# Kernel tuning notes

Hardware: AMD Instinct MI355X
Metric: run time of the kernel (lower is better)

The kernel has to match this reference:

```python
import jax, jax.numpy as jnp
import numpy as np

SIGMA = 0.1  # kernel-point influence radius (KPConv linear correlation)


def setup_inputs() -> dict:
    key = jax.random.key(0)
    k1, k2, k3, k4, k5 = jax.random.split(key, 5)
    N, K, KP, CIN, COUT = 65536, 32, 15, 64, 128
    pos = jax.random.uniform(k1, (N, 3), dtype=jnp.float32)
    feats = jax.random.normal(k2, (N, CIN), dtype=jnp.float32)
    kernel_points = jax.random.normal(k3, (KP, 3), dtype=jnp.float32) * 0.05
    weights = jax.random.normal(k4, (KP, CIN, COUT), dtype=jnp.float32) / np.sqrt(KP * CIN)
    neighbors = jax.random.randint(k5, (N, K), 0, N, dtype=jnp.int64)
    return {"pos": pos, "feats": feats, "kernel_points": kernel_points,
            "weights": weights, "neighbors": neighbors}


def reference(pos, feats, kernel_points, weights, neighbors):
    # pos: [N,3], feats: [N,Cin], kernel_points: [Kp,3],
    # weights: [Kp,Cin,Cout], neighbors: [N,K] int
    neigh_pos = pos[neighbors]                      # [N,K,3] irregular gather
    rel = neigh_pos - pos[:, None, :]               # [N,K,3]
    # distance from each relative neighbor offset to each kernel point
    d = rel[:, :, None, :] - kernel_points[None, None, :, :]   # [N,K,Kp,3]
    dist = jnp.sqrt(jnp.sum(d * d, axis=-1))        # [N,K,Kp]
    infl = jnp.maximum(0.0, 1.0 - dist / SIGMA)     # linear correlation
    neigh_feat = feats[neighbors]                   # [N,K,Cin] irregular gather
    # per-kernel-point weighted neighbor aggregation, then projection
    weighted = jnp.einsum('njk,njc->nkc', infl, neigh_feat)    # [N,Kp,Cin]
    out = jnp.einsum('nkc,kcd->nd', weighted, weights)         # [N,Cout]
    return out
```

## Files before the change

### kernel.cpp

```cpp
#include <hip/hip_runtime.h>

#define NPTS  65536
#define KNB   32
#define KPn   15
#define CIN   64
#define COUT  128
#define MPTS  16
#define THREADS 256
#define TPB   4
#define WSTRIDE 968
#define BCAP  48
#define RCAP  96
#define NTILE 8
#define KSTEPS 30
#define WELEMS (NTILE * KSTEPS * 64 * 8)

typedef __attribute__((ext_vector_type(8))) short short8;
typedef __attribute__((ext_vector_type(4))) float f32x4;

__device__ __forceinline__ unsigned int f2bf(float f) {
    union { float f; unsigned int i; } v; v.f = f;
    return (v.i + 0x7fffu + ((v.i >> 16) & 1u)) >> 16;
}

__global__ void wtrans_kernel(const float* __restrict__ w,
                              const float* __restrict__ kpts,
                              unsigned short* __restrict__ wTf,
                              float4* __restrict__ kpq_out) {
    const int d = blockIdx.x * 256 + threadIdx.x;
    if (d < WELEMS) {
        const int j    = d & 7;
        const int lane = (d >> 3) & 63;
        const int ks   = (d >> 9) % KSTEPS;
        const int t    = d / (KSTEPS * 512);
        const int f    = ks * 32 + (lane >> 4) * 8 + j;
        const int cg   = f / 120;
        const int rem  = f - cg * 120;
        const int orig = (rem >> 3) * 64 + cg * 8 + (rem & 7);
        const int n    = t * 16 + (lane & 15);
        wTf[d] = (unsigned short)f2bf(w[(size_t)orig * COUT + n]);
    }
    if (blockIdx.x == 0 && threadIdx.x < 16) {
        const int k = threadIdx.x;
        if (k < KPn) {
            const float x = kpts[k * 3 + 0];
            const float y = kpts[k * 3 + 1];
            const float z = kpts[k * 3 + 2];
            kpq_out[k] = make_float4(x, y, z, x * x + y * y + z * z);
        } else {
            float mx = 0.f;
            for (int i = 0; i < KPn; ++i) {
                const float x = kpts[i * 3 + 0];
                const float y = kpts[i * 3 + 1];
                const float z = kpts[i * 3 + 2];
                mx = fmaxf(mx, x * x + y * y + z * z);
            }
            const float R = 0.1f + sqrtf(mx);
            kpq_out[15] = make_float4(R * R, 0.f, 0.f, 0.f);
        }
    }
}

__global__ __launch_bounds__(THREADS, 4) void kpconv_kernel(
    const float* __restrict__ pos,
    const float* __restrict__ feats,
    const unsigned short* __restrict__ wTf,
    const float4* __restrict__ kpq_in,
    const int*   __restrict__ neighbors,
    float*       __restrict__ out)
{
    __shared__ unsigned short wl[MPTS * WSTRIDE];
    __shared__ unsigned int  bpk[MPTS][BCAP];
    __shared__ int    bcnt[MPTS];
    __shared__ float  cposf[MPTS * 3];
    __shared__ float4 kpq[KPn];
    __shared__ float  rlx[RCAP], rly[RCAP], rlz[RCAP], rld[RCAP];
    __shared__ unsigned int rsl[RCAP];
    __shared__ int    nact;
    __shared__ float  R2s;

    const int tid = threadIdx.x;

    if (tid < KPn) kpq[tid] = kpq_in[tid];
    if (tid == KPn) R2s = kpq_in[15].x;

    for (int t8 = 0; t8 < TPB; ++t8) {
        const int n0 = (blockIdx.x * TPB + t8) * MPTS;

        if (tid < MPTS) bcnt[tid] = 0;
        if (tid == THREADS - 1) nact = 0;
        if (tid < MPTS * 3) cposf[tid] = pos[(size_t)n0 * 3 + tid];
        __syncthreads();

        {
            const float R2 = R2s;
            #pragma unroll
            for (int it = 0; it < 2; ++it) {
                const int s  = tid + it * THREADS;
                const int p  = s >> 5;
                const int nb = neighbors[(size_t)n0 * KNB + s];
                const float rx = pos[(size_t)nb * 3 + 0] - cposf[p * 3 + 0];
                const float ry = pos[(size_t)nb * 3 + 1] - cposf[p * 3 + 1];
                const float rz = pos[(size_t)nb * 3 + 2] - cposf[p * 3 + 2];
                const float d2r = rx * rx + ry * ry + rz * rz;
                if (d2r < R2) {
                    const int idx = atomicAdd(&nact, 1);
                    if (idx < RCAP) {
                        rlx[idx] = rx; rly[idx] = ry; rlz[idx] = rz; rld[idx] = d2r;
                        rsl[idx] = ((unsigned int)p << 16) | (unsigned int)nb;
                    }
                }
            }
        }
        __syncthreads();

        {
            const int E = min(nact, RCAP);
            for (int u = tid; u < E * 16; u += THREADS) {
                const int e = u >> 4;
                const int k = u & 15;
                if (k < KPn) {
                    const float4 kp  = kpq[k];
                    const float  d2r = rld[e];
                    const float dot = rlx[e] * kp.x + rly[e] * kp.y + rlz[e] * kp.z;
                    if (dot > 0.5f * (d2r - 0.01f + kp.w)) {
                        const float d2 = fmaxf(d2r - 2.f * dot + kp.w, 0.f);
                        const float w  = 1.0f - 10.0f * sqrtf(d2);
                        const unsigned int wq = (unsigned int)(w * 4095.0f + 0.5f);
                        const unsigned int sl = rsl[e];
                        const int p = (int)(sl >> 16);
                        const int idx = atomicAdd(&bcnt[p], 1);
                        if (idx < BCAP)
                            bpk[p][idx] = ((sl & 0xFFFFu) << 16) |
                                          ((unsigned int)k << 12) | wq;
                    }
                }
            }
        }
        __syncthreads();

        #pragma unroll
        for (int it = 0; it < 8; ++it) {
            const int wi = tid + it * THREADS;
            const int cg = wi & 7;
            const int k  = (wi >> 3) & 15;
            const int p  = wi >> 7;
            if (k < KPn) {
                float a0=0.f,a1=0.f,a2=0.f,a3=0.f,a4=0.f,a5=0.f,a6=0.f,a7=0.f;
                const int cnt = min(bcnt[p], BCAP);
                for (int e = 0; e < cnt; ++e) {
                    const unsigned int id = bpk[p][e];
                    if (((id >> 12) & 15u) == (unsigned int)k) {
                        const float wv = (float)(id & 4095u) * (1.0f / 4095.0f);
                        const float* fr = feats + (size_t)(id >> 16) * CIN + cg * 8;
                        const float4 f0 = *(const float4*)fr;
                        const float4 f1 = *(const float4*)(fr + 4);
                        a0 += wv * f0.x; a1 += wv * f0.y; a2 += wv * f0.z; a3 += wv * f0.w;
                        a4 += wv * f1.x; a5 += wv * f1.y; a6 += wv * f1.z; a7 += wv * f1.w;
                    }
                }
                uint4 u;
                u.x = f2bf(a0) | (f2bf(a1) << 16);
                u.y = f2bf(a2) | (f2bf(a3) << 16);
                u.z = f2bf(a4) | (f2bf(a5) << 16);
                u.w = f2bf(a6) | (f2bf(a7) << 16);
                *(uint4*)(wl + p * WSTRIDE + cg * 120 + k * 8) = u;
            }
        }
        __syncthreads();

        {
            const int wave = tid >> 6;
            const int lane = tid & 63;
            const int m    = lane & 15;
            const int q    = lane >> 4;

            f32x4 acc0 = {0.f, 0.f, 0.f, 0.f};
            f32x4 acc1 = {0.f, 0.f, 0.f, 0.f};

            const unsigned short* ap = wl + m * WSTRIDE + q * 8;
            const short8* bp0 = (const short8*)wTf + (size_t)(2 * wave) * KSTEPS * 64 + lane;
            const short8* bp1 = bp0 + (size_t)KSTEPS * 64;

            #pragma unroll 5
            for (int ks = 0; ks < KSTEPS; ++ks, ap += 32) {
                const short8 a  = *(const short8*)ap;
                const short8 b0 = bp0[ks * 64];
                const short8 b1 = bp1[ks * 64];
                acc0 = __builtin_amdgcn_mfma_f32_16x16x32_bf16(a, b0, acc0, 0, 0, 0);
                acc1 = __builtin_amdgcn_mfma_f32_16x16x32_bf16(a, b1, acc1, 0, 0, 0);
            }

            const int nb0 = wave * 32;
            #pragma unroll
            for (int r = 0; r < 4; ++r) {
                const size_t row = (size_t)(n0 + q * 4 + r) * COUT;
                out[row + nb0 + m]      = acc0[r];
                out[row + nb0 + 16 + m] = acc1[r];
            }
        }
    }
}

extern "C" void kernel_launch(void* const* d_in, const int* in_sizes, int n_in,
                              void* d_out, int out_size, void* d_ws, size_t ws_size,
                              hipStream_t stream) {
    const float* pos       = (const float*)d_in[0];
    const float* feats     = (const float*)d_in[1];
    const float* kpts      = (const float*)d_in[2];
    const float* weights   = (const float*)d_in[3];
    const int*   neighbors = (const int*)d_in[4];
    float*       out       = (float*)d_out;
    unsigned short* wTf    = (unsigned short*)d_ws;
    float4* kpq            = (float4*)((char*)d_ws + WELEMS * 2);

    wtrans_kernel<<<(WELEMS + 255) / 256, 256, 0, stream>>>(weights, kpts, wTf, kpq);
    kpconv_kernel<<<NPTS / (MPTS * TPB), THREADS, 0, stream>>>(
        pos, feats, wTf, kpq, neighbors, out);
}
```

Before: 145.3 us.

## Process 32 points per block in one pass instead of looping over 16-point tiles

Removes the per-block loop over four 16-point tiles. Each block now handles 32 points once, with 2048 blocks instead of 1024, and the candidate buffer capacity is raised to match. In the MFMA stage each wave computes two M-tiles, so every B fragment loaded from global weights is reused across 32 rows instead of 16. This halves weight traffic per point, but LDS use per block roughly doubles and the launch-bounds occupancy hint drops from 4 to 2.

Measured after the change: 160.1 us. 10.2% more time.

```diff
diff --git a/kernel.cpp b/kernel.cpp
--- a/kernel.cpp
+++ b/kernel.cpp
@@ -5,12 +5,11 @@
 #define KPn   15
 #define CIN   64
 #define COUT  128
-#define MPTS  16
+#define MPTS  32
 #define THREADS 256
-#define TPB   4
 #define WSTRIDE 968
 #define BCAP  48
-#define RCAP  96
+#define RCAP  160
 #define NTILE 8
 #define KSTEPS 30
 #define WELEMS (NTILE * KSTEPS * 64 * 8)
@@ -61,7 +60,7 @@
     }
 }
 
-__global__ __launch_bounds__(THREADS, 4) void kpconv_kernel(
+__global__ __launch_bounds__(THREADS, 2) void kpconv_kernel(
     const float* __restrict__ pos,
     const float* __restrict__ feats,
     const unsigned short* __restrict__ wTf,
@@ -80,124 +79,129 @@
     __shared__ float  R2s;
 
     const int tid = threadIdx.x;
+    const int n0  = blockIdx.x * MPTS;
 
     if (tid < KPn) kpq[tid] = kpq_in[tid];
     if (tid == KPn) R2s = kpq_in[15].x;
-
-    for (int t8 = 0; t8 < TPB; ++t8) {
-        const int n0 = (blockIdx.x * TPB + t8) * MPTS;
-
-        if (tid < MPTS) bcnt[tid] = 0;
-        if (tid == THREADS - 1) nact = 0;
-        if (tid < MPTS * 3) cposf[tid] = pos[(size_t)n0 * 3 + tid];
-        __syncthreads();
-
-        {
-            const float R2 = R2s;
-            #pragma unroll
-            for (int it = 0; it < 2; ++it) {
-                const int s  = tid + it * THREADS;
-                const int p  = s >> 5;
-                const int nb = neighbors[(size_t)n0 * KNB + s];
-                const float rx = pos[(size_t)nb * 3 + 0] - cposf[p * 3 + 0];
-                const float ry = pos[(size_t)nb * 3 + 1] - cposf[p * 3 + 1];
-                const float rz = pos[(size_t)nb * 3 + 2] - cposf[p * 3 + 2];
-                const float d2r = rx * rx + ry * ry + rz * rz;
-                if (d2r < R2) {
-                    const int idx = atomicAdd(&nact, 1);
-                    if (idx < RCAP) {
-                        rlx[idx] = rx; rly[idx] = ry; rlz[idx] = rz; rld[idx] = d2r;
-                        rsl[idx] = ((unsigned int)p << 16) | (unsigned int)nb;
-                    }
+    if (tid < MPTS) bcnt[tid] = 0;
+    if (tid == THREADS - 1) nact = 0;
+    if (tid < MPTS * 3) cposf[tid] = pos[(size_t)n0 * 3 + tid];
+    __syncthreads();
+
+    {
+        const float R2 = R2s;
+        #pragma unroll
+        for (int it = 0; it < MPTS * KNB / THREADS; ++it) {
+            const int s  = tid + it * THREADS;
+            const int p  = s >> 5;
+            const int nb = neighbors[(size_t)n0 * KNB + s];
+            const float rx = pos[(size_t)nb * 3 + 0] - cposf[p * 3 + 0];
+            const float ry = pos[(size_t)nb * 3 + 1] - cposf[p * 3 + 1];
+            const float rz = pos[(size_t)nb * 3 + 2] - cposf[p * 3 + 2];
+            const float d2r = rx * rx + ry * ry + rz * rz;
+            if (d2r < R2) {
+                const int idx = atomicAdd(&nact, 1);
+                if (idx < RCAP) {
+                    rlx[idx] = rx; rly[idx] = ry; rlz[idx] = rz; rld[idx] = d2r;
+                    rsl[idx] = ((unsigned int)p << 16) | (unsigned int)nb;
                 }
             }
         }
-        __syncthreads();
-
-        {
-            const int E = min(nact, RCAP);
-            for (int u = tid; u < E * 16; u += THREADS) {
-                const int e = u >> 4;
-                const int k = u & 15;
-                if (k < KPn) {
-                    const float4 kp  = kpq[k];
-                    const float  d2r = rld[e];
-                    const float dot = rlx[e] * kp.x + rly[e] * kp.y + rlz[e] * kp.z;
-                    if (dot > 0.5f * (d2r - 0.01f + kp.w)) {
-                        const float d2 = fmaxf(d2r - 2.f * dot + kp.w, 0.f);
-                        const float w  = 1.0f - 10.0f * sqrtf(d2);
-                        const unsigned int wq = (unsigned int)(w * 4095.0f + 0.5f);
-                        const unsigned int sl = rsl[e];
-                        const int p = (int)(sl >> 16);
-                        const int idx = atomicAdd(&bcnt[p], 1);
-                        if (idx < BCAP)
-                            bpk[p][idx] = ((sl & 0xFFFFu) << 16) |
-                                          ((unsigned int)k << 12) | wq;
-                    }
+    }
+    __syncthreads();
+
+    {
+        const int E = min(nact, RCAP);
+        for (int u = tid; u < E * 16; u += THREADS) {
+            const int e = u >> 4;
+            const int k = u & 15;
+            if (k < KPn) {
+                const float4 kp  = kpq[k];
+                const float  d2r = rld[e];
+                const float dot = rlx[e] * kp.x + rly[e] * kp.y + rlz[e] * kp.z;
+                if (dot > 0.5f * (d2r - 0.01f + kp.w)) {
+                    const float d2 = fmaxf(d2r - 2.f * dot + kp.w, 0.f);
+                    const float w  = 1.0f - 10.0f * sqrtf(d2);
+                    const unsigned int wq = (unsigned int)(w * 4095.0f + 0.5f);
+                    const unsigned int sl = rsl[e];
+                    const int p = (int)(sl >> 16);
+                    const int idx = atomicAdd(&bcnt[p], 1);
+                    if (idx < BCAP)
+                        bpk[p][idx] = ((sl & 0xFFFFu) << 16) |
+                                      ((unsigned int)k << 12) | wq;
                 }
             }
         }
-        __syncthreads();
-
+    }
+    __syncthreads();
+
+    #pragma unroll
+    for (int it = 0; it < 16; ++it) {
+        const int wi = tid + it * THREADS;
+        const int cg = wi & 7;
+        const int k  = (wi >> 3) & 15;
+        const int p  = wi >> 7;
+        if (k < KPn) {
+            float a0=0.f,a1=0.f,a2=0.f,a3=0.f,a4=0.f,a5=0.f,a6=0.f,a7=0.f;
+            const int cnt = min(bcnt[p], BCAP);
+            for (int e = 0; e < cnt; ++e) {
+                const unsigned int id = bpk[p][e];
+                if (((id >> 12) & 15u) == (unsigned int)k) {
+                    const float wv = (float)(id & 4095u) * (1.0f / 4095.0f);
+                    const float* fr = feats + (size_t)(id >> 16) * CIN + cg * 8;
+                    const float4 f0 = *(const float4*)fr;
+                    const float4 f1 = *(const float4*)(fr + 4);
+                    a0 += wv * f0.x; a1 += wv * f0.y; a2 += wv * f0.z; a3 += wv * f0.w;
+                    a4 += wv * f1.x; a5 += wv * f1.y; a6 += wv * f1.z; a7 += wv * f1.w;
+                }
+            }
+            uint4 u;
+            u.x = f2bf(a0) | (f2bf(a1) << 16);
+            u.y = f2bf(a2) | (f2bf(a3) << 16);
+            u.z = f2bf(a4) | (f2bf(a5) << 16);
+            u.w = f2bf(a6) | (f2bf(a7) << 16);
+            *(uint4*)(wl + p * WSTRIDE + cg * 120 + k * 8) = u;
+        }
+    }
+    __syncthreads();
+
+    {
+        const int wave = tid >> 6;
+        const int lane = tid & 63;
+        const int m    = lane & 15;
+        const int q    = lane >> 4;
+
+        f32x4 acc00 = {0.f,0.f,0.f,0.f};
+        f32x4 acc01 = {0.f,0.f,0.f,0.f};
+        f32x4 acc10 = {0.f,0.f,0.f,0.f};
+        f32x4 acc11 = {0.f,0.f,0.f,0.f};
+
+        const unsigned short* a0p = wl + m * WSTRIDE + q * 8;
+        const unsigned short* a1p = a0p + 16 * WSTRIDE;
+        const short8* bp0 = (const short8*)wTf + (size_t)(2 * wave) * KSTEPS * 64 + lane;
+        const short8* bp1 = bp0 + (size_t)KSTEPS * 64;
+
+        #pragma unroll 5
+        for (int ks = 0; ks < KSTEPS; ++ks, a0p += 32, a1p += 32) {
+            const short8 a0 = *(const short8*)a0p;
+            const short8 a1 = *(const short8*)a1p;
+            const short8 b0 = bp0[ks * 64];
+            const short8 b1 = bp1[ks * 64];
+            acc00 = __builtin_amdgcn_mfma_f32_16x16x32_bf16(a0, b0, acc00, 0, 0, 0);
+            acc01 = __builtin_amdgcn_mfma_f32_16x16x32_bf16(a0, b1, acc01, 0, 0, 0);
+            acc10 = __builtin_amdgcn_mfma_f32_16x16x32_bf16(a1, b0, acc10, 0, 0, 0);
+            acc11 = __builtin_amdgcn_mfma_f32_16x16x32_bf16(a1, b1, acc11, 0, 0, 0);
+        }
+
+        const int c0 = 2 * wave * 16 + m;
         #pragma unroll
-        for (int it = 0; it < 8; ++it) {
-            const int wi = tid + it * THREADS;
-            const int cg = wi & 7;
-            const int k  = (wi >> 3) & 15;
-            const int p  = wi >> 7;
-            if (k < KPn) {
-                float a0=0.f,a1=0.f,a2=0.f,a3=0.f,a4=0.f,a5=0.f,a6=0.f,a7=0.f;
-                const int cnt = min(bcnt[p], BCAP);
-                for (int e = 0; e < cnt; ++e) {
-                    const unsigned int id = bpk[p][e];
-                    if (((id >> 12) & 15u) == (unsigned int)k) {
-                        const float wv = (float)(id & 4095u) * (1.0f / 4095.0f);
-                        const float* fr = feats + (size_t)(id >> 16) * CIN + cg * 8;
-                        const float4 f0 = *(const float4*)fr;
-                        const float4 f1 = *(const float4*)(fr + 4);
-                        a0 += wv * f0.x; a1 += wv * f0.y; a2 += wv * f0.z; a3 += wv * f0.w;
-                        a4 += wv * f1.x; a5 += wv * f1.y; a6 += wv * f1.z; a7 += wv * f1.w;
-                    }
-                }
-                uint4 u;
-                u.x = f2bf(a0) | (f2bf(a1) << 16);
-                u.y = f2bf(a2) | (f2bf(a3) << 16);
-                u.z = f2bf(a4) | (f2bf(a5) << 16);
-                u.w = f2bf(a6) | (f2bf(a7) << 16);
-                *(uint4*)(wl + p * WSTRIDE + cg * 120 + k * 8) = u;
-            }
-        }
-        __syncthreads();
-
-        {
-            const int wave = tid >> 6;
-            const int lane = tid & 63;
-            const int m    = lane & 15;
-            const int q    = lane >> 4;
-
-            f32x4 acc0 = {0.f, 0.f, 0.f, 0.f};
-            f32x4 acc1 = {0.f, 0.f, 0.f, 0.f};
-
-            const unsigned short* ap = wl + m * WSTRIDE + q * 8;
-            const short8* bp0 = (const short8*)wTf + (size_t)(2 * wave) * KSTEPS * 64 + lane;
-            const short8* bp1 = bp0 + (size_t)KSTEPS * 64;
-
-            #pragma unroll 5
-            for (int ks = 0; ks < KSTEPS; ++ks, ap += 32) {
-                const short8 a  = *(const short8*)ap;
-                const short8 b0 = bp0[ks * 64];
-                const short8 b1 = bp1[ks * 64];
-                acc0 = __builtin_amdgcn_mfma_f32_16x16x32_bf16(a, b0, acc0, 0, 0, 0);
-                acc1 = __builtin_amdgcn_mfma_f32_16x16x32_bf16(a, b1, acc1, 0, 0, 0);
-            }
-
-            const int nb0 = wave * 32;
-            #pragma unroll
-            for (int r = 0; r < 4; ++r) {
-                const size_t row = (size_t)(n0 + q * 4 + r) * COUT;
-                out[row + nb0 + m]      = acc0[r];
-                out[row + nb0 + 16 + m] = acc1[r];
-            }
+        for (int r = 0; r < 4; ++r) {
+            const size_t row0 = (size_t)(n0 + q * 4 + r) * COUT;
+            const size_t row1 = (size_t)(n0 + 16 + q * 4 + r) * COUT;
+            out[row0 + c0]      = acc00[r];
+            out[row0 + c0 + 16] = acc01[r];
+            out[row1 + c0]      = acc10[r];
+            out[row1 + c0 + 16] = acc11[r];
         }
     }
 }
@@ -215,6 +219,6 @@
     float4* kpq            = (float4*)((char*)d_ws + WELEMS * 2);
 
     wtrans_kernel<<<(WELEMS + 255) / 256, 256, 0, stream>>>(weights, kpts, wTf, kpq);
-    kpconv_kernel<<<NPTS / (MPTS * TPB), THREADS, 0, stream>>>(
+    kpconv_kernel<<<NPTS / MPTS, THREADS, 0, stream>>>(
         pos, feats, wTf, kpq, neighbors, out);
 }
```

## Use 512-thread blocks, one 16-point tile per block, one MFMA tile per wave

Applied to the files above, without the earlier changes.

The kernel stops looping over 4 point tiles per block. Each block now handles a single 16-point tile with 512 threads, launching 4x more blocks, and each of the 8 waves computes one 16-column output tile instead of two. The aim is more parallelism and latency hiding across the gather and MFMA phases, and removing the serial per-tile loop. In exchange the kpq setup is repeated per block, there is more block launch overhead, and each wave has less MFMA work to amortize its A-fragment LDS loads.

Result: faster. 138.2 us (-4.9%).

```diff
diff --git a/kernel.cpp b/kernel.cpp
--- a/kernel.cpp
+++ b/kernel.cpp
@@ -6,8 +6,7 @@
 #define CIN   64
 #define COUT  128
 #define MPTS  16
-#define THREADS 256
-#define TPB   4
+#define THREADS 512
 #define WSTRIDE 968
 #define BCAP  48
 #define RCAP  96
@@ -61,7 +60,7 @@
     }
 }
 
-__global__ __launch_bounds__(THREADS, 4) void kpconv_kernel(
+__global__ __launch_bounds__(THREADS, 8) void kpconv_kernel(
     const float* __restrict__ pos,
     const float* __restrict__ feats,
     const unsigned short* __restrict__ wTf,
@@ -80,125 +79,110 @@
     __shared__ float  R2s;
 
     const int tid = threadIdx.x;
+    const int n0  = blockIdx.x * MPTS;
 
     if (tid < KPn) kpq[tid] = kpq_in[tid];
     if (tid == KPn) R2s = kpq_in[15].x;
-
-    for (int t8 = 0; t8 < TPB; ++t8) {
-        const int n0 = (blockIdx.x * TPB + t8) * MPTS;
-
-        if (tid < MPTS) bcnt[tid] = 0;
-        if (tid == THREADS - 1) nact = 0;
-        if (tid < MPTS * 3) cposf[tid] = pos[(size_t)n0 * 3 + tid];
-        __syncthreads();
-
-        {
-            const float R2 = R2s;
-            #pragma unroll
-            for (int it = 0; it < 2; ++it) {
-                const int s  = tid + it * THREADS;
-                const int p  = s >> 5;
-                const int nb = neighbors[(size_t)n0 * KNB + s];
-                const float rx = pos[(size_t)nb * 3 + 0] - cposf[p * 3 + 0];
-                const float ry = pos[(size_t)nb * 3 + 1] - cposf[p * 3 + 1];
-                const float rz = pos[(size_t)nb * 3 + 2] - cposf[p * 3 + 2];
-                const float d2r = rx * rx + ry * ry + rz * rz;
-                if (d2r < R2) {
-                    const int idx = atomicAdd(&nact, 1);
-                    if (idx < RCAP) {
-                        rlx[idx] = rx; rly[idx] = ry; rlz[idx] = rz; rld[idx] = d2r;
-                        rsl[idx] = ((unsigned int)p << 16) | (unsigned int)nb;
-                    }
+    if (tid < MPTS) bcnt[tid] = 0;
+    if (tid == THREADS - 1) nact = 0;
+    if (tid < MPTS * 3) cposf[tid] = pos[(size_t)n0 * 3 + tid];
+    __syncthreads();
+
+    {
+        const float R2 = R2s;
+        const int s  = tid;
+        const int p  = s >> 5;
+        const int nb = neighbors[(size_t)n0 * KNB + s];
+        const float rx = pos[(size_t)nb * 3 + 0] - cposf[p * 3 + 0];
+        const float ry = pos[(size_t)nb * 3 + 1] - cposf[p * 3 + 1];
+        const float rz = pos[(size_t)nb * 3 + 2] - cposf[p * 3 + 2];
+        const float d2r = rx * rx + ry * ry + rz * rz;
+        if (d2r < R2) {
+            const int idx = atomicAdd(&nact, 1);
+            if (idx < RCAP) {
+                rlx[idx] = rx; rly[idx] = ry; rlz[idx] = rz; rld[idx] = d2r;
+                rsl[idx] = ((unsigned int)p << 16) | (unsigned int)nb;
+            }
+        }
+    }
+    __syncthreads();
+
+    {
+        const int E = min(nact, RCAP);
+        for (int u = tid; u < E * 16; u += THREADS) {
+            const int e = u >> 4;
+            const int k = u & 15;
+            if (k < KPn) {
+                const float4 kp  = kpq[k];
+                const float  d2r = rld[e];
+                const float dot = rlx[e] * kp.x + rly[e] * kp.y + rlz[e] * kp.z;
+                if (dot > 0.5f * (d2r - 0.01f + kp.w)) {
+                    const float d2 = fmaxf(d2r - 2.f * dot + kp.w, 0.f);
+                    const float w  = 1.0f - 10.0f * sqrtf(d2);
+                    const unsigned int wq = (unsigned int)(w * 4095.0f + 0.5f);
+                    const unsigned int sl = rsl[e];
+                    const int p = (int)(sl >> 16);
+                    const int idx = atomicAdd(&bcnt[p], 1);
+                    if (idx < BCAP)
+                        bpk[p][idx] = ((sl & 0xFFFFu) << 16) |
+                                      ((unsigned int)k << 12) | wq;
                 }
             }
         }
-        __syncthreads();
-
-        {
-            const int E = min(nact, RCAP);
-            for (int u = tid; u < E * 16; u += THREADS) {
-                const int e = u >> 4;
-                const int k = u & 15;
-                if (k < KPn) {
-                    const float4 kp  = kpq[k];
-                    const float  d2r = rld[e];
-                    const float dot = rlx[e] * kp.x + rly[e] * kp.y + rlz[e] * kp.z;
-                    if (dot > 0.5f * (d2r - 0.01f + kp.w)) {
-                        const float d2 = fmaxf(d2r - 2.f * dot + kp.w, 0.f);
-                        const float w  = 1.0f - 10.0f * sqrtf(d2);
-                        const unsigned int wq = (unsigned int)(w * 4095.0f + 0.5f);
-                        const unsigned int sl = rsl[e];
-                        const int p = (int)(sl >> 16);
-                        const int idx = atomicAdd(&bcnt[p], 1);
-                        if (idx < BCAP)
-                            bpk[p][idx] = ((sl & 0xFFFFu) << 16) |
-                                          ((unsigned int)k << 12) | wq;
-                    }
+    }
+    __syncthreads();
+
+    #pragma unroll
+    for (int it = 0; it < 4; ++it) {
+        const int wi = tid + it * THREADS;
+        const int cg = wi & 7;
+        const int k  = (wi >> 3) & 15;
+        const int p  = wi >> 7;
+        if (k < KPn) {
+            float a0=0.f,a1=0.f,a2=0.f,a3=0.f,a4=0.f,a5=0.f,a6=0.f,a7=0.f;
+            const int cnt = min(bcnt[p], BCAP);
+            for (int e = 0; e < cnt; ++e) {
+                const unsigned int id = bpk[p][e];
+                if (((id >> 12) & 15u) == (unsigned int)k) {
+                    const float wv = (float)(id & 4095u) * (1.0f / 4095.0f);
+                    const float* fr = feats + (size_t)(id >> 16) * CIN + cg * 8;
+                    const float4 f0 = *(const float4*)fr;
+                    const float4 f1 = *(const float4*)(fr + 4);
+                    a0 += wv * f0.x; a1 += wv * f0.y; a2 += wv * f0.z; a3 += wv * f0.w;
+                    a4 += wv * f1.x; a5 += wv * f1.y; a6 += wv * f1.z; a7 += wv * f1.w;
                 }
             }
-        }
-        __syncthreads();
-
+            uint4 u;
+            u.x = f2bf(a0) | (f2bf(a1) << 16);
+            u.y = f2bf(a2) | (f2bf(a3) << 16);
+            u.z = f2bf(a4) | (f2bf(a5) << 16);
+            u.w = f2bf(a6) | (f2bf(a7) << 16);
+            *(uint4*)(wl + p * WSTRIDE + cg * 120 + k * 8) = u;
+        }
+    }
+    __syncthreads();
+
+    {
+        const int wave = tid >> 6;
+        const int lane = tid & 63;
+        const int m    = lane & 15;
+        const int q    = lane >> 4;
+
+        f32x4 acc = {0.f, 0.f, 0.f, 0.f};
+        const unsigned short* ap = wl + m * WSTRIDE + q * 8;
+        const short8* bp = (const short8*)wTf + (size_t)wave * KSTEPS * 64 + lane;
+
+        #pragma unroll 5
+        for (int ks = 0; ks < KSTEPS; ++ks, ap += 32) {
+            const short8 a = *(const short8*)ap;
+            const short8 b = bp[ks * 64];
+            acc = __builtin_amdgcn_mfma_f32_16x16x32_bf16(a, b, acc, 0, 0, 0);
+        }
+
+        const int c = wave * 16 + m;
         #pragma unroll
-        for (int it = 0; it < 8; ++it) {
-            const int wi = tid + it * THREADS;
-            const int cg = wi & 7;
-            const int k  = (wi >> 3) & 15;
-            const int p  = wi >> 7;
-            if (k < KPn) {
-                float a0=0.f,a1=0.f,a2=0.f,a3=0.f,a4=0.f,a5=0.f,a6=0.f,a7=0.f;
-                const int cnt = min(bcnt[p], BCAP);
-                for (int e = 0; e < cnt; ++e) {
-                    const unsigned int id = bpk[p][e];
-                    if (((id >> 12) & 15u) == (unsigned int)k) {
-                        const float wv = (float)(id & 4095u) * (1.0f / 4095.0f);
-                        const float* fr = feats + (size_t)(id >> 16) * CIN + cg * 8;
-                        const float4 f0 = *(const float4*)fr;
-                        const float4 f1 = *(const float4*)(fr + 4);
-                        a0 += wv * f0.x; a1 += wv * f0.y; a2 += wv * f0.z; a3 += wv * f0.w;
-                        a4 += wv * f1.x; a5 += wv * f1.y; a6 += wv * f1.z; a7 += wv * f1.w;
-                    }
-                }
-                uint4 u;
-                u.x = f2bf(a0) | (f2bf(a1) << 16);
-                u.y = f2bf(a2) | (f2bf(a3) << 16);
-                u.z = f2bf(a4) | (f2bf(a5) << 16);
-                u.w = f2bf(a6) | (f2bf(a7) << 16);
-                *(uint4*)(wl + p * WSTRIDE + cg * 120 + k * 8) = u;
-            }
-        }
-        __syncthreads();
-
-        {
-            const int wave = tid >> 6;
-            const int lane = tid & 63;
-            const int m    = lane & 15;
-            const int q    = lane >> 4;
-
-            f32x4 acc0 = {0.f, 0.f, 0.f, 0.f};
-            f32x4 acc1 = {0.f, 0.f, 0.f, 0.f};
-
-            const unsigned short* ap = wl + m * WSTRIDE + q * 8;
-            const short8* bp0 = (const short8*)wTf + (size_t)(2 * wave) * KSTEPS * 64 + lane;
-            const short8* bp1 = bp0 + (size_t)KSTEPS * 64;
-
-            #pragma unroll 5
-            for (int ks = 0; ks < KSTEPS; ++ks, ap += 32) {
-                const short8 a  = *(const short8*)ap;
-                const short8 b0 = bp0[ks * 64];
-                const short8 b1 = bp1[ks * 64];
-                acc0 = __builtin_amdgcn_mfma_f32_16x16x32_bf16(a, b0, acc0, 0, 0, 0);
-                acc1 = __builtin_amdgcn_mfma_f32_16x16x32_bf16(a, b1, acc1, 0, 0, 0);
-            }
-
-            const int nb0 = wave * 32;
-            #pragma unroll
-            for (int r = 0; r < 4; ++r) {
-                const size_t row = (size_t)(n0 + q * 4 + r) * COUT;
-                out[row + nb0 + m]      = acc0[r];
-                out[row + nb0 + 16 + m] = acc1[r];
-            }
-        }
+        for (int r = 0; r < 4; ++r)
+            out[(size_t)(n0 + q * 4 + r) * COUT + c] = acc[r];
     }
 }
 
@@ -215,6 +199,6 @@
     float4* kpq            = (float4*)((char*)d_ws + WELEMS * 2);
 
     wtrans_kernel<<<(WELEMS + 255) / 256, 256, 0, stream>>>(weights, kpts, wTf, kpq);
-    kpconv_kernel<<<NPTS / (MPTS * TPB), THREADS, 0, stream>>>(
+    kpconv_kernel<<<NPTS / MPTS, THREADS, 0, stream>>>(
         pos, feats, wTf, kpq, neighbors, out);
 }
```
